# Kernel optimization log

Hardware: AMD Instinct MI355X
Metric: run time of the kernel (lower is better)

## Reference

```python
import jax, jax.numpy as jnp
import numpy as np
from jax import lax

DN = ('NCHW', 'OIHW', 'NCHW')
EPS = 1e-8
WINDOW_SIZES = (3, 7, 15, 31, 61)

# Sobel kernels, shape (O=1, I=1, 3, 3)
_SOBEL_X = jnp.array([[-1., 0., 1.], [-2., 0., 2.], [-1., 0., 1.]], dtype=jnp.float32)[None, None]
_SOBEL_Y = jnp.array([[-1., -2., -1.], [0., 0., 0.], [1., 2., 1.]], dtype=jnp.float32)[None, None]


def _conv(x, k):
    return lax.conv_general_dilated(x, k.astype(x.dtype), window_strides=(1, 1),
                                    padding='SAME', dimension_numbers=DN)


def _sobel(x):
    return _conv(x, _SOBEL_X), _conv(x, _SOBEL_Y)


def _box(x, w):
    k = jnp.full((1, 1, w, w), 1.0 / (w * w), dtype=x.dtype)
    return _conv(x, k)


def _grad_loss(v, i, img, window_size):
    # Gradient maps of each image
    gvx, gvy = _sobel(v)
    gix, giy = _sobel(i)
    gfx, gfy = _sobel(img)
    # Local (windowed) gradient energy of each source
    ev = _box(gvx * gvx + gvy * gvy, window_size)
    ei = _box(gix * gix + giy * giy, window_size)
    # Per-pixel source weight favoring the locally more salient source
    wt = ev / (ev + ei + EPS)
    tx = wt * gvx + (1.0 - wt) * gix
    ty = wt * gvy + (1.0 - wt) * giy
    return jnp.mean((gfx - tx) ** 2 + (gfy - ty) ** 2)


def setup_inputs() -> dict:
    key = jax.random.key(0)
    kv, ki, kf = jax.random.split(key, 3)
    shape = (8, 1, 512, 512)
    return {
        'v': jax.random.uniform(kv, shape, dtype=jnp.float32),
        'i': jax.random.uniform(ki, shape, dtype=jnp.float32),
        'img': jax.random.uniform(kf, shape, dtype=jnp.float32),
    }


def reference(v, i, img):
    loss = jnp.asarray(0.0, dtype=v.dtype)
    for ws in WINDOW_SIZES:
        loss = loss + _grad_loss(v, i, img, ws)
    return loss
```

## Files before the change

### kernel.cpp

```cpp
#include <hip/hip_runtime.h>

#define H 512
#define W 512
#define NIMG 8
#define SW 513
#define SAT_PER (SW * SW)
#define NBAND 16
#define BROWS 32

#define PS 576
#define PP (PS * PS)
#define PADY 32
#define PADX 32

typedef float f4 __attribute__((ext_vector_type(4), aligned(4)));

__device__ __forceinline__ f4 ld4(const float* p) {
    return *reinterpret_cast<const f4*>(p);
}

__device__ __forceinline__ float ldz(const float* __restrict__ p, int y, int x) {
    return ((unsigned)y < (unsigned)H && (unsigned)x < (unsigned)W) ? p[y * W + x] : 0.0f;
}

__global__ __launch_bounds__(512) void k_rowscan(const float* __restrict__ v,
                                                 const float* __restrict__ i_,
                                                 float* __restrict__ B) {
    const int bid = blockIdx.x;
    const int n = bid & 7;
    const int t = bid >> 3;
    const int m = t & 1;
    const int y = t >> 1;
    const int x = threadIdx.x;
    const float* src = (m == 0 ? v : i_) + (size_t)n * (H * W);

    float gx, gy;
    {
        float a00 = ldz(src, y - 1, x - 1), a01 = ldz(src, y - 1, x), a02 = ldz(src, y - 1, x + 1);
        float a10 = ldz(src, y,     x - 1),                            a12 = ldz(src, y,     x + 1);
        float a20 = ldz(src, y + 1, x - 1), a21 = ldz(src, y + 1, x), a22 = ldz(src, y + 1, x + 1);
        gx = (a02 - a00) + 2.0f * (a12 - a10) + (a22 - a20);
        gy = (a20 - a00) + 2.0f * (a21 - a01) + (a22 - a02);
    }
    float e = gx * gx + gy * gy;

    const int lane = x & 63, wid = x >> 6;
    float s = e;
    #pragma unroll
    for (int off = 1; off < 64; off <<= 1) {
        float t2 = __shfl_up(s, off, 64);
        if (lane >= off) s += t2;
    }
    __shared__ float wt[8];
    if (lane == 63) wt[wid] = s;
    __syncthreads();
    float o = 0.0f;
    for (int w2 = 0; w2 < wid; ++w2) o += wt[w2];
    float incl = s + o;

    float* row = B + (size_t)(n * 2 + m) * SAT_PER + (size_t)(y + 1) * SW;
    row[x + 1] = incl;
    if (x == 0) row[0] = 0.0f;
}

__global__ __launch_bounds__(576) void k_bandsum(const float* __restrict__ B,
                                                 float* __restrict__ bandsum) {
    const int bid = blockIdx.x;
    const int n = bid & 7;
    const int t = bid >> 3;
    const int m = t & 1;
    const int b = t >> 1;
    const int c = threadIdx.x;
    if (c >= SW) return;
    const int map = n * 2 + m;
    const float* base = B + (size_t)map * SAT_PER + (size_t)(1 + b * BROWS) * SW + c;
    float s = 0.0f;
    #pragma unroll 8
    for (int r = 0; r < BROWS; ++r) s += base[(size_t)r * SW];
    bandsum[((size_t)map * NBAND + b) * SW + c] = s;
}

__global__ __launch_bounds__(576) void k_bandapplyP(const float* __restrict__ B,
                                                    const float* __restrict__ bandsum,
                                                    float* __restrict__ P) {
    const int bid = blockIdx.x;
    const int n = bid & 7;
    const int t = bid >> 3;
    const int m = t & 1;
    const int b = t >> 1;
    const int c = threadIdx.x;
    const int map = n * 2 + m;
    const int x = min(max(c - PADX, 0), W);

    float* Pm = P + (size_t)map * PP;
    const float* Bm = B + (size_t)map * SAT_PER;
    const float* bs = bandsum + (size_t)map * NBAND * SW + x;

    if (b == 0) {
        #pragma unroll
        for (int j = 0; j <= PADY; ++j)
            Pm[(size_t)j * PS + c] = 0.0f;
    }

    float run = 0.0f;
    for (int bb = 0; bb < b; ++bb) run += bs[(size_t)bb * SW];

    const float* Brow = Bm + (size_t)(1 + b * BROWS) * SW + x;
    float* Prow = Pm + (size_t)(PADY + 1 + b * BROWS) * PS + c;
    #pragma unroll 8
    for (int j = 0; j < BROWS; ++j) {
        run += Brow[(size_t)j * SW];
        Prow[(size_t)j * PS] = run;
    }

    if (b == NBAND - 1) {
        float* Ppad = Pm + (size_t)(PADY + 1 + H) * PS + c;
        #pragma unroll
        for (int j = 0; j < PS - (PADY + 1 + H); ++j)
            Ppad[(size_t)j * PS] = run;
    }
}

__device__ __forceinline__ void sobel4(const float* __restrict__ p, int y, int x4,
                                       bool fast, float gx[4], float gy[4]) {
    float r0[6], r1[6], r2[6];
    if (fast) {
        const float* a = p + (size_t)(y - 1) * W + (x4 - 1);
        #pragma unroll
        for (int q = 0; q < 6; ++q) {
            r0[q] = a[q]; r1[q] = a[W + q]; r2[q] = a[2 * W + q];
        }
    } else {
        #pragma unroll
        for (int q = 0; q < 6; ++q) {
            r0[q] = ldz(p, y - 1, x4 - 1 + q);
            r1[q] = ldz(p, y,     x4 - 1 + q);
            r2[q] = ldz(p, y + 1, x4 - 1 + q);
        }
    }
    #pragma unroll
    for (int q = 0; q < 4; ++q) {
        gx[q] = (r0[q + 2] - r0[q]) + 2.0f * (r1[q + 2] - r1[q]) + (r2[q + 2] - r2[q]);
        gy[q] = (r2[q] - r0[q]) + 2.0f * (r2[q + 1] - r0[q + 1]) + (r2[q + 2] - r0[q + 2]);
    }
}

__global__ __launch_bounds__(256) void k_main(const float* __restrict__ v,
                                              const float* __restrict__ i_,
                                              const float* __restrict__ img,
                                              const float* __restrict__ P,
                                              double* __restrict__ partials) {
    const int bid = blockIdx.x;
    const int n = bid & 7;
    const int t = bid >> 3;
    const int tx = t & 3, ty = t >> 2;
    const int col = threadIdx.x & 31, row = threadIdx.x >> 5;
    const int x4 = tx * 128 + col * 4;
    const int y  = ty * 8 + row;

    const float* pv = v   + (size_t)n * (H * W);
    const float* pi = i_  + (size_t)n * (H * W);
    const float* pf = img + (size_t)n * (H * W);
    const float* Pv = P + (size_t)(n * 2 + 0) * PP;
    const float* Pi = P + (size_t)(n * 2 + 1) * PP;

    float gvx[4], gvy[4], gix[4], giy[4], gfx[4], gfy[4];
    const bool fast = (y >= 1 && y <= H - 2 && x4 >= 4 && x4 <= W - 8);
    sobel4(pv, y, x4, fast, gvx, gvy);
    sobel4(pi, y, x4, fast, gix, giy);
    sobel4(pf, y, x4, fast, gfx, gfy);

    float dvx[4], dvy[4], rx[4], ry[4];
    #pragma unroll
    for (int q = 0; q < 4; ++q) {
        dvx[q] = gvx[q] - gix[q];
        dvy[q] = gvy[q] - giy[q];
        rx[q]  = gfx[q] - gix[q];
        ry[q]  = gfy[q] - giy[q];
    }

    const int   radii[5] = {1, 3, 7, 15, 30};
    const float epsw[5]  = {9e-8f, 4.9e-7f, 2.25e-6f, 9.61e-6f, 3.721e-5f};

    float acc = 0.0f;
    #pragma unroll
    for (int k = 0; k < 5; ++k) {
        const int r = radii[k];
        const size_t ro0 = (size_t)(y - r + PADY) * PS;
        const size_t ro1 = (size_t)(y + r + 1 + PADY) * PS;
        const int x0 = x4 - r + PADX;
        const int x1 = x4 + r + 1 + PADX;
        f4 sa = ld4(Pv + ro1 + x1), sb = ld4(Pv + ro0 + x1);
        f4 sc = ld4(Pv + ro1 + x0), sd = ld4(Pv + ro0 + x0);
        f4 ua = ld4(Pi + ro1 + x1), ub = ld4(Pi + ro0 + x1);
        f4 uc = ld4(Pi + ro1 + x0), ud = ld4(Pi + ro0 + x0);
        f4 sv = sa - sb - sc + sd;
        f4 si = ua - ub - uc + ud;
        #pragma unroll
        for (int q = 0; q < 4; ++q) {
            float d  = sv[q] + si[q] + epsw[k];
            float wt = sv[q] * __builtin_amdgcn_rcpf(d);
            float dx = rx[q] - wt * dvx[q];
            float dy = ry[q] - wt * dvy[q];
            acc += dx * dx + dy * dy;
        }
    }

    double a = (double)acc;
    const int lane = threadIdx.x & 63, wid = threadIdx.x >> 6;
    #pragma unroll
    for (int off = 32; off > 0; off >>= 1) a += __shfl_down(a, off, 64);
    __shared__ double red[4];
    if (lane == 0) red[wid] = a;
    __syncthreads();
    if (threadIdx.x == 0)
        partials[bid] = red[0] + red[1] + red[2] + red[3];
}

__global__ __launch_bounds__(256) void k_reduce(const double* __restrict__ partials,
                                                int np, float* __restrict__ out) {
    __shared__ double red[256];
    double s = 0.0;
    for (int idx = threadIdx.x; idx < np; idx += 256) s += partials[idx];
    red[threadIdx.x] = s;
    __syncthreads();
    #pragma unroll
    for (int t = 128; t > 0; t >>= 1) {
        if (threadIdx.x < t) red[threadIdx.x] += red[threadIdx.x + t];
        __syncthreads();
    }
    if (threadIdx.x == 0)
        out[0] = (float)(red[0] / (double)((size_t)NIMG * H * W));
}


extern "C" void kernel_launch(void* const* d_in, const int* in_sizes, int n_in,
                              void* d_out, int out_size, void* d_ws, size_t ws_size,
                              hipStream_t stream) {
    const float* v   = (const float*)d_in[0];
    const float* i_  = (const float*)d_in[1];
    const float* img = (const float*)d_in[2];
    float* out = (float*)d_out;

    float* B         = (float*)d_ws;
    float* bandsum   = B + (size_t)16 * SAT_PER;
    float* P         = bandsum + (size_t)16 * NBAND * SW;
    double* partials = (double*)(P + (size_t)16 * PP);

    k_rowscan<<<dim3(512 * NIMG * 2), dim3(512), 0, stream>>>(v, i_, B);
    k_bandsum<<<dim3(NBAND * NIMG * 2), dim3(576), 0, stream>>>(B, bandsum);
    k_bandapplyP<<<dim3(NBAND * NIMG * 2), dim3(576), 0, stream>>>(B, bandsum, P);
    k_main<<<dim3(2048), dim3(256), 0, stream>>>(v, i_, img, P, partials);
    k_reduce<<<dim3(1), dim3(256), 0, stream>>>(partials, 2048, out);
}
```

Baseline: 56.85 us.

## Fuse row scan and band sums into one LDS-tiled kernel, apply column prefix in place

Merges the per-row Sobel-energy row scan and the band-sum pass into one kernel. Each block handles a 16-row band, computes row prefix sums in a padded shared-memory tile, writes band totals and raw row scans straight into the padded P buffer, and a second kernel adds the column prefix in place. This removes the separate SAT buffer B and one launch, and uses vectorized loads with wave shuffles for the halo. The Sobel loads in the main kernel also become vector loads. Changing PADX and the tile layout risks subtle off-by-one errors in the padded SAT indexing.

```diff
diff --git a/kernel.cpp b/kernel.cpp
--- a/kernel.cpp
+++ b/kernel.cpp
@@ -3,17 +3,20 @@
 #define H 512
 #define W 512
 #define NIMG 8
-#define SW 513
-#define SAT_PER (SW * SW)
-#define NBAND 16
-#define BROWS 32
+#define NBAND 32
+#define BROWS 16
 
 #define PS 576
 #define PP (PS * PS)
 #define PADY 32
-#define PADX 32
+#define PADX 31
+
+#define TSTR 648
 
 typedef float f4 __attribute__((ext_vector_type(4), aligned(4)));
+typedef float f2 __attribute__((ext_vector_type(2), aligned(4)));
+
+__device__ __forceinline__ int phi(int c) { return c + 4 * (c >> 5); }
 
 __device__ __forceinline__ f4 ld4(const float* p) {
     return *reinterpret_cast<const f4*>(p);
@@ -23,101 +26,127 @@
     return ((unsigned)y < (unsigned)H && (unsigned)x < (unsigned)W) ? p[y * W + x] : 0.0f;
 }
 
-__global__ __launch_bounds__(512) void k_rowscan(const float* __restrict__ v,
+__device__ __forceinline__ void loadrow(const float* __restrict__ src, int row,
+                                        int x0, int lane, float w[10]) {
+    f4 a = {0.f, 0.f, 0.f, 0.f}, b = {0.f, 0.f, 0.f, 0.f};
+    if ((unsigned)row < (unsigned)H) {
+        const float* p = src + (size_t)row * W + x0;
+        a = ld4(p);
+        b = ld4(p + 4);
+    }
+    float left = __shfl_up(b[3], 1, 64);
+    if (lane == 0) left = 0.f;
+    float right = __shfl_down(a[0], 1, 64);
+    if (lane == 63) right = 0.f;
+    w[0] = left;
+    w[1] = a[0]; w[2] = a[1]; w[3] = a[2]; w[4] = a[3];
+    w[5] = b[0]; w[6] = b[1]; w[7] = b[2]; w[8] = b[3];
+    w[9] = right;
+}
+
+__global__ __launch_bounds__(512) void k_rowband(const float* __restrict__ v,
                                                  const float* __restrict__ i_,
-                                                 float* __restrict__ B) {
-    const int bid = blockIdx.x;
-    const int n = bid & 7;
-    const int t = bid >> 3;
-    const int m = t & 1;
-    const int y = t >> 1;
-    const int x = threadIdx.x;
-    const float* src = (m == 0 ? v : i_) + (size_t)n * (H * W);
-
-    float gx, gy;
-    {
-        float a00 = ldz(src, y - 1, x - 1), a01 = ldz(src, y - 1, x), a02 = ldz(src, y - 1, x + 1);
-        float a10 = ldz(src, y,     x - 1),                            a12 = ldz(src, y,     x + 1);
-        float a20 = ldz(src, y + 1, x - 1), a21 = ldz(src, y + 1, x), a22 = ldz(src, y + 1, x + 1);
-        gx = (a02 - a00) + 2.0f * (a12 - a10) + (a22 - a20);
-        gy = (a20 - a00) + 2.0f * (a21 - a01) + (a22 - a02);
-    }
-    float e = gx * gx + gy * gy;
-
-    const int lane = x & 63, wid = x >> 6;
-    float s = e;
-    #pragma unroll
-    for (int off = 1; off < 64; off <<= 1) {
-        float t2 = __shfl_up(s, off, 64);
-        if (lane >= off) s += t2;
-    }
-    __shared__ float wt[8];
-    if (lane == 63) wt[wid] = s;
-    __syncthreads();
-    float o = 0.0f;
-    for (int w2 = 0; w2 < wid; ++w2) o += wt[w2];
-    float incl = s + o;
-
-    float* row = B + (size_t)(n * 2 + m) * SAT_PER + (size_t)(y + 1) * SW;
-    row[x + 1] = incl;
-    if (x == 0) row[0] = 0.0f;
-}
-
-__global__ __launch_bounds__(576) void k_bandsum(const float* __restrict__ B,
+                                                 float* __restrict__ P,
                                                  float* __restrict__ bandsum) {
     const int bid = blockIdx.x;
     const int n = bid & 7;
     const int t = bid >> 3;
     const int m = t & 1;
     const int b = t >> 1;
-    const int c = threadIdx.x;
-    if (c >= SW) return;
     const int map = n * 2 + m;
-    const float* base = B + (size_t)map * SAT_PER + (size_t)(1 + b * BROWS) * SW + c;
-    float s = 0.0f;
-    #pragma unroll 8
-    for (int r = 0; r < BROWS; ++r) s += base[(size_t)r * SW];
-    bandsum[((size_t)map * NBAND + b) * SW + c] = s;
-}
-
-__global__ __launch_bounds__(576) void k_bandapplyP(const float* __restrict__ B,
-                                                    const float* __restrict__ bandsum,
-                                                    float* __restrict__ P) {
+    const float* src = (m == 0 ? v : i_) + (size_t)n * (H * W);
+    float* Pm = P + (size_t)map * PP;
+
+    __shared__ float tile[BROWS][TSTR];
+
+    const int tid = threadIdx.x;
+    const int lane = tid & 63, wv = tid >> 6;
+    const int x0 = lane * 8;
+
+    if (b == 0) {
+        const f4 z = {0.f, 0.f, 0.f, 0.f};
+        for (int s = tid; s < 33 * (PS / 4); s += 512) {
+            int j = s / (PS / 4), c4 = s - j * (PS / 4);
+            *reinterpret_cast<f4*>(Pm + (size_t)j * PS + 4 * c4) = z;
+        }
+    }
+
+    #pragma unroll
+    for (int k = 0; k < 2; ++k) {
+        const int j = k * 8 + wv;
+        const int y = b * BROWS + j;
+        float w0[10], w1[10], w2[10];
+        loadrow(src, y - 1, x0, lane, w0);
+        loadrow(src, y,     x0, lane, w1);
+        loadrow(src, y + 1, x0, lane, w2);
+        float e[8];
+        #pragma unroll
+        for (int q = 0; q < 8; ++q) {
+            float gx = (w0[q + 2] - w0[q]) + 2.0f * (w1[q + 2] - w1[q]) + (w2[q + 2] - w2[q]);
+            float gy = (w2[q] - w0[q]) + 2.0f * (w2[q + 1] - w0[q + 1]) + (w2[q + 2] - w0[q + 2]);
+            e[q] = gx * gx + gy * gy;
+        }
+        #pragma unroll
+        for (int q = 1; q < 8; ++q) e[q] += e[q - 1];
+        const float tot = e[7];
+        float s = tot;
+        #pragma unroll
+        for (int off = 1; off < 64; off <<= 1) {
+            float t2 = __shfl_up(s, off, 64);
+            if (lane >= off) s += t2;
+        }
+        const float excl = s - tot;
+        const int pc = phi(32 + x0);
+        #pragma unroll
+        for (int q = 0; q < 8; ++q) tile[j][pc + q] = e[q] + excl;
+    }
+    __syncthreads();
+
+    {
+        const int j = tid >> 5, c = tid & 31;
+        tile[j][phi(c)] = 0.f;
+        tile[j][phi(544 + c)] = tile[j][phi(543)];
+    }
+    __syncthreads();
+
+    float* bs = bandsum + ((size_t)map * NBAND + b) * PS;
+    for (int c = tid; c < PS; c += 512) {
+        float s = 0.f;
+        #pragma unroll
+        for (int j = 0; j < BROWS; ++j) s += tile[j][phi(c)];
+        bs[c] = s;
+    }
+
+    for (int s4 = tid; s4 < BROWS * (PS / 4); s4 += 512) {
+        int j = s4 / (PS / 4), c4 = s4 - j * (PS / 4);
+        f4 val = *reinterpret_cast<const f4*>(&tile[j][phi(4 * c4)]);
+        *reinterpret_cast<f4*>(Pm + (size_t)(PADY + 1 + b * BROWS + j) * PS + 4 * c4) = val;
+    }
+}
+
+__global__ __launch_bounds__(576) void k_colapply(float* __restrict__ P,
+                                                  const float* __restrict__ bandsum) {
     const int bid = blockIdx.x;
     const int n = bid & 7;
     const int t = bid >> 3;
     const int m = t & 1;
     const int b = t >> 1;
+    const int map = n * 2 + m;
     const int c = threadIdx.x;
-    const int map = n * 2 + m;
-    const int x = min(max(c - PADX, 0), W);
-
-    float* Pm = P + (size_t)map * PP;
-    const float* Bm = B + (size_t)map * SAT_PER;
-    const float* bs = bandsum + (size_t)map * NBAND * SW + x;
-
-    if (b == 0) {
-        #pragma unroll
-        for (int j = 0; j <= PADY; ++j)
-            Pm[(size_t)j * PS + c] = 0.0f;
-    }
-
-    float run = 0.0f;
-    for (int bb = 0; bb < b; ++bb) run += bs[(size_t)bb * SW];
-
-    const float* Brow = Bm + (size_t)(1 + b * BROWS) * SW + x;
-    float* Prow = Pm + (size_t)(PADY + 1 + b * BROWS) * PS + c;
-    #pragma unroll 8
+    const float* bs = bandsum + (size_t)map * NBAND * PS + c;
+    float run = 0.f;
+    for (int bb = 0; bb < b; ++bb) run += bs[(size_t)bb * PS];
+    float* Pr = P + (size_t)map * PP + (size_t)(PADY + 1 + b * BROWS) * PS + c;
+    #pragma unroll
     for (int j = 0; j < BROWS; ++j) {
-        run += Brow[(size_t)j * SW];
-        Prow[(size_t)j * PS] = run;
-    }
-
+        run += Pr[(size_t)j * PS];
+        Pr[(size_t)j * PS] = run;
+    }
     if (b == NBAND - 1) {
-        float* Ppad = Pm + (size_t)(PADY + 1 + H) * PS + c;
+        float* Pp = P + (size_t)map * PP + (size_t)(PADY + 1 + H) * PS + c;
         #pragma unroll
         for (int j = 0; j < PS - (PADY + 1 + H); ++j)
-            Ppad[(size_t)j * PS] = run;
+            Pp[(size_t)j * PS] = run;
     }
 }
 
@@ -126,10 +155,12 @@
     float r0[6], r1[6], r2[6];
     if (fast) {
         const float* a = p + (size_t)(y - 1) * W + (x4 - 1);
-        #pragma unroll
-        for (int q = 0; q < 6; ++q) {
-            r0[q] = a[q]; r1[q] = a[W + q]; r2[q] = a[2 * W + q];
-        }
+        f4 A = ld4(a);             f2 Ab = *reinterpret_cast<const f2*>(a + 4);
+        f4 Bv = ld4(a + W);        f2 Bb = *reinterpret_cast<const f2*>(a + W + 4);
+        f4 Cv = ld4(a + 2 * W);    f2 Cb = *reinterpret_cast<const f2*>(a + 2 * W + 4);
+        r0[0]=A[0];  r0[1]=A[1];  r0[2]=A[2];  r0[3]=A[3];  r0[4]=Ab[0]; r0[5]=Ab[1];
+        r1[0]=Bv[0]; r1[1]=Bv[1]; r1[2]=Bv[2]; r1[3]=Bv[3]; r1[4]=Bb[0]; r1[5]=Bb[1];
+        r2[0]=Cv[0]; r2[1]=Cv[1]; r2[2]=Cv[2]; r2[3]=Cv[3]; r2[4]=Cb[0]; r2[5]=Cb[1];
     } else {
         #pragma unroll
         for (int q = 0; q < 6; ++q) {
@@ -242,14 +273,12 @@
     const float* img = (const float*)d_in[2];
     float* out = (float*)d_out;
 
-    float* B         = (float*)d_ws;
-    float* bandsum   = B + (size_t)16 * SAT_PER;
-    float* P         = bandsum + (size_t)16 * NBAND * SW;
-    double* partials = (double*)(P + (size_t)16 * PP);
-
-    k_rowscan<<<dim3(512 * NIMG * 2), dim3(512), 0, stream>>>(v, i_, B);
-    k_bandsum<<<dim3(NBAND * NIMG * 2), dim3(576), 0, stream>>>(B, bandsum);
-    k_bandapplyP<<<dim3(NBAND * NIMG * 2), dim3(576), 0, stream>>>(B, bandsum, P);
+    float* P         = (float*)d_ws;
+    float* bandsum   = P + (size_t)16 * PP;
+    double* partials = (double*)(bandsum + (size_t)16 * NBAND * PS);
+
+    k_rowband<<<dim3(NBAND * NIMG * 2), dim3(512), 0, stream>>>(v, i_, P, bandsum);
+    k_colapply<<<dim3(NBAND * NIMG * 2), dim3(576), 0, stream>>>(P, bandsum);
     k_main<<<dim3(2048), dim3(256), 0, stream>>>(v, i_, img, P, partials);
     k_reduce<<<dim3(1), dim3(256), 0, stream>>>(partials, 2048, out);
 }
```

After: 49.40 us. 13.1% less time.
